# Performance work log

Hardware: AMD Instinct MI355X
Metric: run time of the kernel (lower is better)

## Reference

```python
import jax, jax.numpy as jnp
import numpy as np

# Module hyperparameters (init kwargs)
QUALITY_W = 1.0
UNCERT_W = 0.5
STEP_PEN = 0.1
EARLY_BONUS = 0.5
LATE_PEN = 0.3
ORTHO_W = 1.0

B = 8388608  # batch
MAX_STEPS = 20


def setup_inputs() -> dict:
    key = jax.random.key(0)
    ks = jax.random.split(key, 6)
    return {
        "current_quality": jax.random.uniform(ks[0], (B,), dtype=jnp.float32),
        "previous_quality": jax.random.uniform(ks[1], (B,), dtype=jnp.float32),
        "uncertainty": jax.random.uniform(ks[2], (B,), dtype=jnp.float32),
        "action": jax.random.randint(ks[3], (B,), 0, 2, dtype=jnp.int32),
        "step_count": jax.random.uniform(ks[4], (B,), dtype=jnp.float32) * MAX_STEPS,
        "final_quality": jax.random.uniform(ks[5], (B,), dtype=jnp.float32),
        "alpha": jnp.float32(1.0),
        "beta": jnp.float32(1.0),
        "gamma": jnp.float32(1.0),
        "max_steps": MAX_STEPS,
    }


def _corr(x, y):
    # torch .std() is unbiased (ddof=1)
    xm = x - x.mean()
    ym = y - y.mean()
    cov = (xm * ym).mean()
    sx = jnp.sqrt((xm * xm).sum() / (x.shape[0] - 1)) + 1e-8
    sy = jnp.sqrt((ym * ym).sum() / (y.shape[0] - 1)) + 1e-8
    return cov / (sx * sy)


def reference(current_quality, previous_quality, uncertainty, action, step_count,
              final_quality, alpha, beta, gamma, max_steps):
    ms = jnp.float32(max_steps)
    u = uncertainty

    # short-term: quality improvement
    r_short = current_quality - previous_quality

    # mid-term (vectorized form of the per-sample python loop)
    stop_r = jnp.where(u < 0.3, EARLY_BONUS, jnp.where(u > 0.7, -EARLY_BONUS, 0.0))
    cont_r = jnp.where(u > 0.5, UNCERT_W * u, -UNCERT_W * (1.0 - u))
    cont_r = cont_r - jnp.where(step_count > 0.8 * ms, LATE_PEN, 0.0)
    r_mid = jnp.where(action == 0, stop_r, cont_r) - STEP_PEN * (step_count / ms)
    # original builds r_mid via torch.tensor(list) -> detached from graph
    r_mid = jax.lax.stop_gradient(r_mid)

    # long-term
    r_long = QUALITY_W * final_quality + EARLY_BONUS * (1.0 - step_count / ms)

    total_reward = alpha * r_short + beta * r_mid + gamma * r_long

    c_sm = _corr(r_short, r_mid)
    c_sl = _corr(r_short, r_long)
    c_ml = _corr(r_mid, r_long)
    ortho_loss = ORTHO_W * (c_sm ** 2 + c_sl ** 2 + c_ml ** 2)

    return total_reward, ortho_loss, r_short, r_mid, r_long
```

## Files before the change

kernel.cpp:

```cpp
#include <hip/hip_runtime.h>
#include <math.h>

constexpr int    N       = 8388608;
constexpr int    THREADS = 256;
constexpr int    BLOCKS  = 2048;
constexpr int    VEC     = 4;
constexpr int    ITERS   = N / (BLOCKS * THREADS * VEC);
constexpr int    NSUMS   = 9;

__device__ inline double wave_reduce(double x) {
#pragma unroll
    for (int off = 32; off > 0; off >>= 1)
        x += __shfl_down(x, off, 64);
    return x;
}

__device__ inline void elem_compute(float cq, float pq, float u, int a, float sc, float fq,
                                    float ms, float inv_ms,
                                    float alpha, float beta, float gamma,
                                    float& rs, float& rm, float& rl, float& tot)
{
    rs = cq - pq;
    float stop_r = (u < 0.3f) ? 0.5f : ((u > 0.7f) ? -0.5f : 0.0f);
    float cont = (u > 0.5f) ? (0.5f * u) : (-0.5f * (1.0f - u));
    cont -= (sc > 0.8f * ms) ? 0.3f : 0.0f;
    float t = sc * inv_ms;
    rm = ((a == 0) ? stop_r : cont) - 0.1f * t;
    rl = fq + 0.5f * (1.0f - t);
    tot = alpha * rs + beta * rm + gamma * rl;
}

__global__ __launch_bounds__(THREADS) void reward_main(
    const float* __restrict__ cq, const float* __restrict__ pq,
    const float* __restrict__ un, const int*  __restrict__ ac,
    const float* __restrict__ sc, const float* __restrict__ fq,
    const float* __restrict__ alpha_p, const float* __restrict__ beta_p,
    const float* __restrict__ gamma_p, const int* __restrict__ ms_p,
    float* __restrict__ out, double* __restrict__ partials)
{
    const float alpha = alpha_p[0], beta = beta_p[0], gamma = gamma_p[0];
    const float ms = (float)ms_p[0];
    const float inv_ms = 1.0f / ms;

    const float4* cq4 = (const float4*)cq;
    const float4* pq4 = (const float4*)pq;
    const float4* un4 = (const float4*)un;
    const int4*   ac4 = (const int4*)ac;
    const float4* sc4 = (const float4*)sc;
    const float4* fq4 = (const float4*)fq;

    double acc[NSUMS];
#pragma unroll
    for (int s = 0; s < NSUMS; ++s) acc[s] = 0.0;

    const int tid  = blockIdx.x * THREADS + threadIdx.x;
    const int lane = threadIdx.x & 63;

#pragma unroll
    for (int it = 0; it < ITERS; ++it) {
        const int idx4 = tid + it * (BLOCKS * THREADS);
        float4 q = cq4[idx4];
        float4 p = pq4[idx4];
        float4 u = un4[idx4];
        int4   a = ac4[idx4];
        float4 s = sc4[idx4];
        float4 f = fq4[idx4];

        float qc[4] = {q.x, q.y, q.z, q.w};
        float pc[4] = {p.x, p.y, p.z, p.w};
        float uc[4] = {u.x, u.y, u.z, u.w};
        int   av[4] = {a.x, a.y, a.z, a.w};
        float sv[4] = {s.x, s.y, s.z, s.w};
        float fv[4] = {f.x, f.y, f.z, f.w};

        float rs[4], rm[4], rl[4], tt[4];
#pragma unroll
        for (int k = 0; k < 4; ++k) {
            elem_compute(qc[k], pc[k], uc[k], av[k], sv[k], fv[k],
                         ms, inv_ms, alpha, beta, gamma,
                         rs[k], rm[k], rl[k], tt[k]);
            double ds = (double)rs[k], dm = (double)rm[k], dl = (double)rl[k];
            acc[0] += ds;      acc[1] += dm;      acc[2] += dl;
            acc[3] += ds * ds; acc[4] += dm * dm; acc[5] += dl * dl;
            acc[6] += ds * dm; acc[7] += ds * dl; acc[8] += dm * dl;
        }

        ((float4*)out)[idx4] = make_float4(tt[0], tt[1], tt[2], tt[3]);

        const int b = idx4 * 4;

        float s0n = __shfl_down(rs[0], 1, 64);
        float s1n = __shfl_down(rs[1], 1, 64);
        float s2n = __shfl_down(rs[2], 1, 64);
        float m0n = __shfl_down(rm[0], 1, 64);
        float m1n = __shfl_down(rm[1], 1, 64);
        float m2n = __shfl_down(rm[2], 1, 64);
        float l0n = __shfl_down(rl[0], 1, 64);
        float l1n = __shfl_down(rl[1], 1, 64);
        float l2n = __shfl_down(rl[2], 1, 64);

        if (lane < 63) {
            *(float4*)(out +     N + 4 + b) = make_float4(rs[3], s0n, s1n, s2n);
            *(float4*)(out + 2 * N + 4 + b) = make_float4(rm[3], m0n, m1n, m2n);
            *(float4*)(out + 3 * N + 4 + b) = make_float4(rl[3], l0n, l1n, l2n);
        }
        if (lane == 0) {
            out[    N + 1 + b] = rs[0]; out[    N + 2 + b] = rs[1]; out[    N + 3 + b] = rs[2];
            out[2 * N + 1 + b] = rm[0]; out[2 * N + 2 + b] = rm[1]; out[2 * N + 3 + b] = rm[2];
            out[3 * N + 1 + b] = rl[0]; out[3 * N + 2 + b] = rl[1]; out[3 * N + 3 + b] = rl[2];
        }
        if (lane == 63) {
            out[    N + 4 + b] = rs[3];
            out[2 * N + 4 + b] = rm[3];
            out[3 * N + 4 + b] = rl[3];
        }
    }

    __shared__ double red[NSUMS][THREADS / 64];
    const int wave = threadIdx.x >> 6;
#pragma unroll
    for (int s = 0; s < NSUMS; ++s) {
        double w = wave_reduce(acc[s]);
        if (lane == 0) red[s][wave] = w;
    }
    __syncthreads();
    if (threadIdx.x == 0) {
#pragma unroll
        for (int s = 0; s < NSUMS; ++s) {
            double t = 0.0;
#pragma unroll
            for (int w = 0; w < THREADS / 64; ++w) t += red[s][w];
            partials[blockIdx.x * NSUMS + s] = t;
        }
    }
}

__global__ __launch_bounds__(256) void reward_finish(const double* __restrict__ partials,
                                                     float* __restrict__ out)
{
    double loc[NSUMS];
#pragma unroll
    for (int s = 0; s < NSUMS; ++s) loc[s] = 0.0;
    for (int i = threadIdx.x; i < BLOCKS; i += 256) {
#pragma unroll
        for (int s = 0; s < NSUMS; ++s) loc[s] += partials[i * NSUMS + s];
    }
    __shared__ double red[NSUMS][4];
    const int lane = threadIdx.x & 63;
    const int wave = threadIdx.x >> 6;
#pragma unroll
    for (int s = 0; s < NSUMS; ++s) {
        double w = wave_reduce(loc[s]);
        if (lane == 0) red[s][wave] = w;
    }
    __syncthreads();
    if (threadIdx.x == 0) {
        double S[NSUMS];
#pragma unroll
        for (int s = 0; s < NSUMS; ++s)
            S[s] = red[s][0] + red[s][1] + red[s][2] + red[s][3];

        const double n = (double)N;
        double mx = S[0] / n, mm = S[1] / n, ml = S[2] / n;
        double cov_sm = S[6] / n - mx * mm;
        double cov_sl = S[7] / n - mx * ml;
        double cov_ml = S[8] / n - mm * ml;
        double sdS = sqrt((S[3] - n * mx * mx) / (n - 1.0)) + 1e-8;
        double sdM = sqrt((S[4] - n * mm * mm) / (n - 1.0)) + 1e-8;
        double sdL = sqrt((S[5] - n * ml * ml) / (n - 1.0)) + 1e-8;
        double c1 = cov_sm / (sdS * sdM);
        double c2 = cov_sl / (sdS * sdL);
        double c3 = cov_ml / (sdM * sdL);
        out[N] = (float)(c1 * c1 + c2 * c2 + c3 * c3);
    }
}

extern "C" void kernel_launch(void* const* d_in, const int* in_sizes, int n_in,
                              void* d_out, int out_size, void* d_ws, size_t ws_size,
                              hipStream_t stream)
{
    const float* cq   = (const float*)d_in[0];
    const float* pq   = (const float*)d_in[1];
    const float* un   = (const float*)d_in[2];
    const int*   ac   = (const int*)d_in[3];
    const float* sc   = (const float*)d_in[4];
    const float* fq   = (const float*)d_in[5];
    const float* alp  = (const float*)d_in[6];
    const float* bet  = (const float*)d_in[7];
    const float* gam  = (const float*)d_in[8];
    const int*   msp  = (const int*)d_in[9];
    float*  out      = (float*)d_out;
    double* partials = (double*)d_ws;

    reward_main<<<BLOCKS, THREADS, 0, stream>>>(cq, pq, un, ac, sc, fq,
                                                alp, bet, gam, msp, out, partials);
    reward_finish<<<1, 256, 0, stream>>>(partials, out);
}
```

Before: 302.9 us.

## Process 8 elements per thread, hoist all loads, use nontemporal stores

Each thread now handles two 8-element chunks and issues all 24 vector loads for both chunks before any compute, so more memory requests are in flight per thread. Output stores switch to nontemporal vector stores to avoid polluting cache with write-only data, and the shuffle-based misaligned store pattern is adapted to 8-element chunks. Launch bounds add a minimum-occupancy hint. Register pressure rises from holding all loaded data at once, and the access pattern per wave changes from interleaved float4 to two consecutive float4s per lane.

```diff
diff --git a/kernel.cpp b/kernel.cpp
--- a/kernel.cpp
+++ b/kernel.cpp
@@ -4,9 +4,18 @@
 constexpr int    N       = 8388608;
 constexpr int    THREADS = 256;
 constexpr int    BLOCKS  = 2048;
-constexpr int    VEC     = 4;
-constexpr int    ITERS   = N / (BLOCKS * THREADS * VEC);
+constexpr int    CHUNK   = 8;
+constexpr int    ITERS   = N / (BLOCKS * THREADS * CHUNK);
 constexpr int    NSUMS   = 9;
+
+static_assert(ITERS == 2, "grid math");
+
+using f32x4 = __attribute__((ext_vector_type(4))) float;
+
+__device__ inline void nt_store4(float* p, float a, float b, float c, float d) {
+    f32x4 v = {a, b, c, d};
+    __builtin_nontemporal_store(v, (f32x4*)p);
+}
 
 __device__ inline double wave_reduce(double x) {
 #pragma unroll
@@ -30,7 +39,70 @@
     tot = alpha * rs + beta * rm + gamma * rl;
 }
 
-__global__ __launch_bounds__(THREADS) void reward_main(
+__device__ inline void process_chunk(
+    float4 qa, float4 qb, float4 pa, float4 pb,
+    float4 ua, float4 ub, int4 aa, int4 ab,
+    float4 sa, float4 sb, float4 fa, float4 fb,
+    int chunk, int lane,
+    float ms, float inv_ms, float alpha, float beta, float gamma,
+    float* __restrict__ out, double (&acc)[NSUMS])
+{
+    float qc[8] = {qa.x, qa.y, qa.z, qa.w, qb.x, qb.y, qb.z, qb.w};
+    float pc[8] = {pa.x, pa.y, pa.z, pa.w, pb.x, pb.y, pb.z, pb.w};
+    float uc[8] = {ua.x, ua.y, ua.z, ua.w, ub.x, ub.y, ub.z, ub.w};
+    int   av[8] = {aa.x, aa.y, aa.z, aa.w, ab.x, ab.y, ab.z, ab.w};
+    float sv[8] = {sa.x, sa.y, sa.z, sa.w, sb.x, sb.y, sb.z, sb.w};
+    float fv[8] = {fa.x, fa.y, fa.z, fa.w, fb.x, fb.y, fb.z, fb.w};
+
+    float rs[8], rm[8], rl[8], tt[8];
+#pragma unroll
+    for (int k = 0; k < 8; ++k) {
+        elem_compute(qc[k], pc[k], uc[k], av[k], sv[k], fv[k],
+                     ms, inv_ms, alpha, beta, gamma,
+                     rs[k], rm[k], rl[k], tt[k]);
+        double ds = (double)rs[k], dm = (double)rm[k], dl = (double)rl[k];
+        acc[0] += ds;      acc[1] += dm;      acc[2] += dl;
+        acc[3] += ds * ds; acc[4] += dm * dm; acc[5] += dl * dl;
+        acc[6] += ds * dm; acc[7] += ds * dl; acc[8] += dm * dl;
+    }
+
+    const int b = chunk * CHUNK;
+
+    nt_store4(out + b,     tt[0], tt[1], tt[2], tt[3]);
+    nt_store4(out + b + 4, tt[4], tt[5], tt[6], tt[7]);
+
+    nt_store4(out +     N + 4 + b, rs[3], rs[4], rs[5], rs[6]);
+    nt_store4(out + 2 * N + 4 + b, rm[3], rm[4], rm[5], rm[6]);
+    nt_store4(out + 3 * N + 4 + b, rl[3], rl[4], rl[5], rl[6]);
+
+    float sn0 = __shfl_down(rs[0], 1, 64);
+    float sn1 = __shfl_down(rs[1], 1, 64);
+    float sn2 = __shfl_down(rs[2], 1, 64);
+    float mn0 = __shfl_down(rm[0], 1, 64);
+    float mn1 = __shfl_down(rm[1], 1, 64);
+    float mn2 = __shfl_down(rm[2], 1, 64);
+    float ln0 = __shfl_down(rl[0], 1, 64);
+    float ln1 = __shfl_down(rl[1], 1, 64);
+    float ln2 = __shfl_down(rl[2], 1, 64);
+
+    if (lane < 63) {
+        nt_store4(out +     N + 8 + b, rs[7], sn0, sn1, sn2);
+        nt_store4(out + 2 * N + 8 + b, rm[7], mn0, mn1, mn2);
+        nt_store4(out + 3 * N + 8 + b, rl[7], ln0, ln1, ln2);
+    }
+    if (lane == 0) {
+        out[    N + 1 + b] = rs[0]; out[    N + 2 + b] = rs[1]; out[    N + 3 + b] = rs[2];
+        out[2 * N + 1 + b] = rm[0]; out[2 * N + 2 + b] = rm[1]; out[2 * N + 3 + b] = rm[2];
+        out[3 * N + 1 + b] = rl[0]; out[3 * N + 2 + b] = rl[1]; out[3 * N + 3 + b] = rl[2];
+    }
+    if (lane == 63) {
+        out[    N + 8 + b] = rs[7];
+        out[2 * N + 8 + b] = rm[7];
+        out[3 * N + 8 + b] = rl[7];
+    }
+}
+
+__global__ __launch_bounds__(THREADS, 4) void reward_main(
     const float* __restrict__ cq, const float* __restrict__ pq,
     const float* __restrict__ un, const int*  __restrict__ ac,
     const float* __restrict__ sc, const float* __restrict__ fq,
@@ -56,65 +128,29 @@
     const int tid  = blockIdx.x * THREADS + threadIdx.x;
     const int lane = threadIdx.x & 63;
 
-#pragma unroll
-    for (int it = 0; it < ITERS; ++it) {
-        const int idx4 = tid + it * (BLOCKS * THREADS);
-        float4 q = cq4[idx4];
-        float4 p = pq4[idx4];
-        float4 u = un4[idx4];
-        int4   a = ac4[idx4];
-        float4 s = sc4[idx4];
-        float4 f = fq4[idx4];
-
-        float qc[4] = {q.x, q.y, q.z, q.w};
-        float pc[4] = {p.x, p.y, p.z, p.w};
-        float uc[4] = {u.x, u.y, u.z, u.w};
-        int   av[4] = {a.x, a.y, a.z, a.w};
-        float sv[4] = {s.x, s.y, s.z, s.w};
-        float fv[4] = {f.x, f.y, f.z, f.w};
-
-        float rs[4], rm[4], rl[4], tt[4];
-#pragma unroll
-        for (int k = 0; k < 4; ++k) {
-            elem_compute(qc[k], pc[k], uc[k], av[k], sv[k], fv[k],
-                         ms, inv_ms, alpha, beta, gamma,
-                         rs[k], rm[k], rl[k], tt[k]);
-            double ds = (double)rs[k], dm = (double)rm[k], dl = (double)rl[k];
-            acc[0] += ds;      acc[1] += dm;      acc[2] += dl;
-            acc[3] += ds * ds; acc[4] += dm * dm; acc[5] += dl * dl;
-            acc[6] += ds * dm; acc[7] += ds * dl; acc[8] += dm * dl;
-        }
-
-        ((float4*)out)[idx4] = make_float4(tt[0], tt[1], tt[2], tt[3]);
-
-        const int b = idx4 * 4;
-
-        float s0n = __shfl_down(rs[0], 1, 64);
-        float s1n = __shfl_down(rs[1], 1, 64);
-        float s2n = __shfl_down(rs[2], 1, 64);
-        float m0n = __shfl_down(rm[0], 1, 64);
-        float m1n = __shfl_down(rm[1], 1, 64);
-        float m2n = __shfl_down(rm[2], 1, 64);
-        float l0n = __shfl_down(rl[0], 1, 64);
-        float l1n = __shfl_down(rl[1], 1, 64);
-        float l2n = __shfl_down(rl[2], 1, 64);
-
-        if (lane < 63) {
-            *(float4*)(out +     N + 4 + b) = make_float4(rs[3], s0n, s1n, s2n);
-            *(float4*)(out + 2 * N + 4 + b) = make_float4(rm[3], m0n, m1n, m2n);
-            *(float4*)(out + 3 * N + 4 + b) = make_float4(rl[3], l0n, l1n, l2n);
-        }
-        if (lane == 0) {
-            out[    N + 1 + b] = rs[0]; out[    N + 2 + b] = rs[1]; out[    N + 3 + b] = rs[2];
-            out[2 * N + 1 + b] = rm[0]; out[2 * N + 2 + b] = rm[1]; out[2 * N + 3 + b] = rm[2];
-            out[3 * N + 1 + b] = rl[0]; out[3 * N + 2 + b] = rl[1]; out[3 * N + 3 + b] = rl[2];
-        }
-        if (lane == 63) {
-            out[    N + 4 + b] = rs[3];
-            out[2 * N + 4 + b] = rm[3];
-            out[3 * N + 4 + b] = rl[3];
-        }
-    }
+    const int c0 = tid;
+    const int c1 = tid + BLOCKS * THREADS;
+
+    const int i0 = 2 * c0, i1 = 2 * c1;
+
+    float4 Qa0 = cq4[i0], Qb0 = cq4[i0 + 1];
+    float4 Pa0 = pq4[i0], Pb0 = pq4[i0 + 1];
+    float4 Ua0 = un4[i0], Ub0 = un4[i0 + 1];
+    int4   Aa0 = ac4[i0], Ab0 = ac4[i0 + 1];
+    float4 Sa0 = sc4[i0], Sb0 = sc4[i0 + 1];
+    float4 Fa0 = fq4[i0], Fb0 = fq4[i0 + 1];
+
+    float4 Qa1 = cq4[i1], Qb1 = cq4[i1 + 1];
+    float4 Pa1 = pq4[i1], Pb1 = pq4[i1 + 1];
+    float4 Ua1 = un4[i1], Ub1 = un4[i1 + 1];
+    int4   Aa1 = ac4[i1], Ab1 = ac4[i1 + 1];
+    float4 Sa1 = sc4[i1], Sb1 = sc4[i1 + 1];
+    float4 Fa1 = fq4[i1], Fb1 = fq4[i1 + 1];
+
+    process_chunk(Qa0, Qb0, Pa0, Pb0, Ua0, Ub0, Aa0, Ab0, Sa0, Sb0, Fa0, Fb0,
+                  c0, lane, ms, inv_ms, alpha, beta, gamma, out, acc);
+    process_chunk(Qa1, Qb1, Pa1, Pb1, Ua1, Ub1, Aa1, Ab1, Sa1, Sb1, Fa1, Fb1,
+                  c1, lane, ms, inv_ms, alpha, beta, gamma, out, acc);
 
     __shared__ double red[NSUMS][THREADS / 64];
     const int wave = threadIdx.x >> 6;
```

Result: slower. 363.5 us (+20.0%).
